# Kernel tuning notes

Measured on AMD Instinct MI355X. Metric: run time of the kernel, lower is better.

The kernel has to match this reference:

```python
import jax, jax.numpy as jnp
import numpy as np


def setup_inputs() -> dict:
    key = jax.random.key(0)
    ks = jax.random.split(key, 6)
    B, T, U = 4, 160, 80
    De, Dd = 640, 640
    inner, vocab = 640, 1024
    return {
        "enc_state": jax.random.normal(ks[0], (B, T, De), jnp.float32),
        "dec_state": jax.random.normal(ks[1], (B, U, Dd), jnp.float32),
        "W1": jax.random.normal(ks[2], (De + Dd, inner), jnp.float32) * (1.0 / np.sqrt(De + Dd)),
        "b1": jax.random.normal(ks[3], (inner,), jnp.float32) * 0.02,
        "W2": jax.random.normal(ks[4], (inner, vocab), jnp.float32) * (1.0 / np.sqrt(inner)),
        "b2": jax.random.normal(ks[5], (vocab,), jnp.float32) * 0.02,
    }


def reference(enc_state, dec_state, W1, b1, W2, b2):
    # Faithful to: cat([enc tiled over U, dec tiled over T], -1) @ W1 + b1,
    # algebraically split so the [B,T,U,2D] concat is never materialized:
    # cat(e, d) @ W1 == e @ W1[:De] + d @ W1[De:]
    De = enc_state.shape[-1]
    W1_enc, W1_dec = W1[:De], W1[De:]
    enc_proj = jnp.einsum("btd,dh->bth", enc_state, W1_enc)   # [B,T,H]
    dec_proj = jnp.einsum("bud,dh->buh", dec_state, W1_dec)   # [B,U,H]
    # broadcast add over the (T,U) lattice -> [B,T,U,H]
    hidden = jnp.tanh(enc_proj[:, :, None, :] + dec_proj[:, None, :, :] + b1)
    logits = jnp.einsum("btuh,hv->btuv", hidden, W2) + b2     # [B,T,U,V]
    return logits
```

## Files before the change

### kernel.cpp

```cpp
#include <hip/hip_runtime.h>
#include <hip/hip_bf16.h>
#include <cstdint>

#define D_    640
#define V_    1024
#define M_    51200

typedef __bf16 bf16x8 __attribute__((ext_vector_type(8)));
typedef float floatx4 __attribute__((ext_vector_type(4)));

__device__ __forceinline__ void g2l16(const void* g, void* l) {
    __builtin_amdgcn_global_load_lds((const __attribute__((address_space(1))) void*)g,
                                     (__attribute__((address_space(3))) void*)l,
                                     16, 0, 0);
}

__device__ __forceinline__ float fast_tanh(float x) {
    float e = __builtin_amdgcn_exp2f(x * 2.8853900817779268f);
    return 1.0f - 2.0f * __builtin_amdgcn_rcpf(e + 1.0f);
}

__global__ __launch_bounds__(256) void proj_kernel(
    const float* __restrict__ enc, const float* __restrict__ dec,
    const float* __restrict__ W1,
    float* __restrict__ encp, float* __restrict__ decp) {
    __shared__ float As[64][36];
    __shared__ float Ws[32][68];

    const int rt = blockIdx.y;
    const int ct = blockIdx.x;
    const float* Asrc; const float* Wsrc; float* Cdst;
    if (rt < 10) { Asrc = enc + (size_t)rt * 64 * D_;        Wsrc = W1;           Cdst = encp + (size_t)rt * 64 * D_; }
    else         { Asrc = dec + (size_t)(rt - 10) * 64 * D_; Wsrc = W1 + D_ * D_; Cdst = decp + (size_t)(rt - 10) * 64 * D_; }

    const int tid = threadIdx.x;
    const int ar = tid >> 2,  ac = (tid & 3) * 8;
    const int wr2 = tid >> 3, wc2 = (tid & 7) * 8;
    const int tr = tid >> 4,  tc = tid & 15;

    float acc[4][4] = {};
    for (int k0 = 0; k0 < D_; k0 += 32) {
        __syncthreads();
        *(floatx4*)&As[ar][ac]       = *(const floatx4*)&Asrc[(size_t)ar * D_ + k0 + ac];
        *(floatx4*)&As[ar][ac + 4]   = *(const floatx4*)&Asrc[(size_t)ar * D_ + k0 + ac + 4];
        *(floatx4*)&Ws[wr2][wc2]     = *(const floatx4*)&Wsrc[(size_t)(k0 + wr2) * D_ + ct * 64 + wc2];
        *(floatx4*)&Ws[wr2][wc2 + 4] = *(const floatx4*)&Wsrc[(size_t)(k0 + wr2) * D_ + ct * 64 + wc2 + 4];
        __syncthreads();
#pragma unroll
        for (int kk = 0; kk < 32; kk++) {
            floatx4 w = *(const floatx4*)&Ws[kk][tc * 4];
            float a0 = As[tr * 4 + 0][kk], a1 = As[tr * 4 + 1][kk];
            float a2 = As[tr * 4 + 2][kk], a3 = As[tr * 4 + 3][kk];
#pragma unroll
            for (int j = 0; j < 4; j++) {
                acc[0][j] += a0 * w[j]; acc[1][j] += a1 * w[j];
                acc[2][j] += a2 * w[j]; acc[3][j] += a3 * w[j];
            }
        }
    }
#pragma unroll
    for (int i = 0; i < 4; i++) {
        floatx4 v = { acc[i][0], acc[i][1], acc[i][2], acc[i][3] };
        *(floatx4*)&Cdst[(size_t)(tr * 4 + i) * D_ + ct * 64 + tc * 4] = v;
    }
}

__global__ __launch_bounds__(256) void w2t_kernel(
    const float* __restrict__ W2, __bf16* __restrict__ W2t) {
    __shared__ __bf16 tile[32][33];
    const int vt = blockIdx.x;
    const int kt = blockIdx.y;
    const int tx = threadIdx.x & 31, ty = threadIdx.x >> 5;
#pragma unroll
    for (int i = 0; i < 4; i++)
        tile[ty + i * 8][tx] = (__bf16)W2[(size_t)(kt * 32 + ty + i * 8) * V_ + vt * 32 + tx];
    __syncthreads();
#pragma unroll
    for (int i = 0; i < 4; i++)
        W2t[(size_t)(vt * 32 + ty + i * 8) * D_ + kt * 32 + tx] = tile[tx][ty + i * 8];
}

__global__ __launch_bounds__(256, 2) void joint_kernel(
    const float* __restrict__ encp, const float* __restrict__ decp,
    const float* __restrict__ b1, const __bf16* __restrict__ W2t,
    const float* __restrict__ b2, float* __restrict__ C) {
    __shared__ __align__(128) char lds[49152];

    const int bid = blockIdx.x;
    const int swz = (bid & 7) * 200 + (bid >> 3);
    const int mt = swz >> 2, nt = swz & 3;
    const int m0 = mt * 128, n0 = nt * 256;

    const int tid = threadIdx.x;
    const int w = tid >> 6, l = tid & 63;
    const int lr = l & 15, lk = l >> 4;

    char* ldsp = (char*)lds;

    const unsigned bsc = (unsigned)(((tid & 3) ^ ((tid >> 4) & 3)) * 16);
    const char* Wb = (const char*)W2t + (size_t)(n0 + (tid >> 2)) * 1280 + bsc;
    const unsigned bdst = (unsigned)(16384 + tid * 16);

    const int pr = tid >> 1;
    const int kh = (tid & 1) * 16;
    const int R  = m0 + pr;
    const int bt = R / 80;
    const int uu = R - bt * 80;
    const int drw = (bt / 160) * 80 + uu;
    const float* ep = encp + (size_t)bt * D_ + kh;
    const float* dp = decp + (size_t)drw * D_ + kh;
    const float* bp = b1 + kh;
    const int ps = (tid & 1) * 2;
    const unsigned psw = (unsigned)((pr >> 2) & 3);
    const unsigned pw0 = (unsigned)(pr * 64 + ((ps ^ psw) * 16));
    const unsigned pw1 = (unsigned)(pr * 64 + (((ps + 1) ^ psw) * 16));

    const unsigned sx = (unsigned)((lk ^ ((lr >> 2) & 3)) * 16);

    floatx4 acc[8][4] = {};

#define STAGE_B(BUF, T) do { \
    const char* _s = Wb + (size_t)(T) * 64; \
    char* _d = ldsp + bdst + (BUF) * 16384; \
    g2l16(_s,                 _d); \
    g2l16(_s + 64 * 1280,     _d + 4096); \
    g2l16(_s + 128 * 1280,    _d + 8192); \
    g2l16(_s + 192 * 1280,    _d + 12288); \
  } while (0)

#define LOAD_EDC(T) do { \
    const float* _e = ep + (T) * 32; const float* _d = dp + (T) * 32; \
    const float* _c = bp + (T) * 32; \
    _Pragma("unroll") for (int q = 0; q < 4; ++q) { \
      eD[q] = *(const floatx4*)(_e + q * 4); \
      dD[q] = *(const floatx4*)(_d + q * 4); \
      cD[q] = *(const floatx4*)(_c + q * 4); \
    } } while (0)

#define PRODUCE_A(BUF) do { \
    bf16x8 h0, h1; \
    _Pragma("unroll") for (int q = 0; q < 4; ++q) { \
      _Pragma("unroll") for (int i2 = 0; i2 < 4; ++i2) { \
        float t_ = fast_tanh(eD[q][i2] + dD[q][i2] + cD[q][i2]); \
        if (q < 2) h0[q * 4 + i2] = (__bf16)t_; else h1[(q - 2) * 4 + i2] = (__bf16)t_; \
      } } \
    *(bf16x8*)(ldsp + (BUF) * 8192 + pw0) = h0; \
    *(bf16x8*)(ldsp + (BUF) * 8192 + pw1) = h1; \
  } while (0)

    {
        floatx4 eD[4], dD[4], cD[4];
        STAGE_B(0, 0);
        LOAD_EDC(0);
        PRODUCE_A(0);
    }
    __syncthreads();

#pragma unroll 1
    for (int t = 0; t < 20; ++t) {
        const int buf = t & 1, nb = buf ^ 1;
        floatx4 eD[4], dD[4], cD[4];
        if (t < 19) {
            STAGE_B(nb, t + 1);
            LOAD_EDC(t + 1);
        }
        bf16x8 af[8], bfr[4];
#pragma unroll
        for (int i = 0; i < 8; ++i)
            af[i] = *(const bf16x8*)(ldsp + buf * 8192 + (i * 16 + lr) * 64 + sx);
#pragma unroll
        for (int j = 0; j < 4; ++j)
            bfr[j] = *(const bf16x8*)(ldsp + 16384 + buf * 16384 + (w * 64 + j * 16 + lr) * 64 + sx);
#pragma unroll
        for (int i = 0; i < 8; ++i)
#pragma unroll
            for (int j = 0; j < 4; ++j)
                acc[i][j] = __builtin_amdgcn_mfma_f32_16x16x32_bf16(af[i], bfr[j], acc[i][j], 0, 0, 0);
        if (t < 19) {
            PRODUCE_A(nb);
        }
        __syncthreads();
    }

#pragma unroll
    for (int j = 0; j < 4; ++j) {
        const int col = n0 + w * 64 + j * 16 + lr;
        const float bj = b2[col];
#pragma unroll
        for (int i = 0; i < 8; ++i) {
            const int row = m0 + i * 16 + lk * 4;
            float* Cp = C + (size_t)row * V_ + col;
#pragma unroll
            for (int rg = 0; rg < 4; ++rg)
                Cp[(size_t)rg * V_] = acc[i][j][rg] + bj;
        }
    }
#undef STAGE_B
#undef LOAD_EDC
#undef PRODUCE_A
}

extern "C" void kernel_launch(void* const* d_in, const int* in_sizes, int n_in,
                              void* d_out, int out_size, void* d_ws, size_t ws_size,
                              hipStream_t stream) {
    const float* enc = (const float*)d_in[0];
    const float* dec = (const float*)d_in[1];
    const float* W1  = (const float*)d_in[2];
    const float* b1  = (const float*)d_in[3];
    const float* W2  = (const float*)d_in[4];
    const float* b2  = (const float*)d_in[5];
    float* out = (float*)d_out;

    char* ws = (char*)d_ws;
    float*  encp = (float*)ws;
    float*  decp = (float*)(ws + 1638400);
    __bf16* W2t  = (__bf16*)(ws + 1638400 + 819200);

    proj_kernel<<<dim3(10, 15), 256, 0, stream>>>(enc, dec, W1, encp, decp);
    w2t_kernel<<<dim3(32, 20), 256, 0, stream>>>(W2, W2t);
    joint_kernel<<<1600, 256, 0, stream>>>(encp, decp, b1, W2t, b2, out);
}
```

Before: 343.6 us.

## Halve joint M tile, double K step, fold b1 into encoder projection

The joint GEMM tile shrinks from 128 to 64 rows, doubling the grid to 3200 blocks, and the K step per iteration grows from 32 to 64. The LDS layout and XOR swizzle are widened to 128-byte rows, and the buffer grows to 80 KB. b1 is now added once in the projection kernel instead of being loaded and added in every joint block. This aims to cut per-iteration barrier overhead and bias traffic, and to give more blocks for latency hiding. In exchange, each output row needs twice as many W2 tile loads per MFMA, and the larger LDS use may limit occupancy.

Measured after the change: 334.7 us. 2.6% less time.

```diff
diff --git a/kernel.cpp b/kernel.cpp
--- a/kernel.cpp
+++ b/kernel.cpp
@@ -22,16 +22,17 @@
 
 __global__ __launch_bounds__(256) void proj_kernel(
     const float* __restrict__ enc, const float* __restrict__ dec,
-    const float* __restrict__ W1,
+    const float* __restrict__ W1, const float* __restrict__ b1,
     float* __restrict__ encp, float* __restrict__ decp) {
     __shared__ float As[64][36];
     __shared__ float Ws[32][68];
 
     const int rt = blockIdx.y;
     const int ct = blockIdx.x;
+    const bool is_enc = (rt < 10);
     const float* Asrc; const float* Wsrc; float* Cdst;
-    if (rt < 10) { Asrc = enc + (size_t)rt * 64 * D_;        Wsrc = W1;           Cdst = encp + (size_t)rt * 64 * D_; }
-    else         { Asrc = dec + (size_t)(rt - 10) * 64 * D_; Wsrc = W1 + D_ * D_; Cdst = decp + (size_t)(rt - 10) * 64 * D_; }
+    if (is_enc) { Asrc = enc + (size_t)rt * 64 * D_;        Wsrc = W1;           Cdst = encp + (size_t)rt * 64 * D_; }
+    else        { Asrc = dec + (size_t)(rt - 10) * 64 * D_; Wsrc = W1 + D_ * D_; Cdst = decp + (size_t)(rt - 10) * 64 * D_; }
 
     const int tid = threadIdx.x;
     const int ar = tid >> 2,  ac = (tid & 3) * 8;
@@ -58,9 +59,12 @@
             }
         }
     }
+    floatx4 bv = {0.f, 0.f, 0.f, 0.f};
+    if (is_enc) bv = *(const floatx4*)&b1[ct * 64 + tc * 4];
 #pragma unroll
     for (int i = 0; i < 4; i++) {
-        floatx4 v = { acc[i][0], acc[i][1], acc[i][2], acc[i][3] };
+        floatx4 v = { acc[i][0] + bv[0], acc[i][1] + bv[1],
+                      acc[i][2] + bv[2], acc[i][3] + bv[3] };
         *(floatx4*)&Cdst[(size_t)(tr * 4 + i) * D_ + ct * 64 + tc * 4] = v;
     }
 }
@@ -82,14 +86,14 @@
 
 __global__ __launch_bounds__(256, 2) void joint_kernel(
     const float* __restrict__ encp, const float* __restrict__ decp,
-    const float* __restrict__ b1, const __bf16* __restrict__ W2t,
-    const float* __restrict__ b2, float* __restrict__ C) {
-    __shared__ __align__(128) char lds[49152];
+    const __bf16* __restrict__ W2t, const float* __restrict__ b2,
+    float* __restrict__ C) {
+    __shared__ __align__(128) char lds[81920];
 
     const int bid = blockIdx.x;
-    const int swz = (bid & 7) * 200 + (bid >> 3);
+    const int swz = (bid & 7) * 400 + (bid >> 3);
     const int mt = swz >> 2, nt = swz & 3;
-    const int m0 = mt * 128, n0 = nt * 256;
+    const int m0 = mt * 64, n0 = nt * 256;
 
     const int tid = threadIdx.x;
     const int w = tid >> 6, l = tid & 63;
@@ -97,51 +101,49 @@
 
     char* ldsp = (char*)lds;
 
-    const unsigned bsc = (unsigned)(((tid & 3) ^ ((tid >> 4) & 3)) * 16);
-    const char* Wb = (const char*)W2t + (size_t)(n0 + (tid >> 2)) * 1280 + bsc;
-    const unsigned bdst = (unsigned)(16384 + tid * 16);
-
-    const int pr = tid >> 1;
-    const int kh = (tid & 1) * 16;
+    const char* Wb = (const char*)W2t
+        + (size_t)(n0 + (tid >> 3)) * 1280
+        + (unsigned)((((tid & 7) ^ ((tid >> 3) & 7)) * 16));
+    const unsigned bdst = 16384u + (unsigned)tid * 16u;
+
+    const int pr = tid >> 2;
+    const int kq = tid & 3;
     const int R  = m0 + pr;
     const int bt = R / 80;
     const int uu = R - bt * 80;
     const int drw = (bt / 160) * 80 + uu;
-    const float* ep = encp + (size_t)bt * D_ + kh;
-    const float* dp = decp + (size_t)drw * D_ + kh;
-    const float* bp = b1 + kh;
-    const int ps = (tid & 1) * 2;
-    const unsigned psw = (unsigned)((pr >> 2) & 3);
-    const unsigned pw0 = (unsigned)(pr * 64 + ((ps ^ psw) * 16));
-    const unsigned pw1 = (unsigned)(pr * 64 + (((ps + 1) ^ psw) * 16));
-
-    const unsigned sx = (unsigned)((lk ^ ((lr >> 2) & 3)) * 16);
-
-    floatx4 acc[8][4] = {};
+    const float* ep = encp + (size_t)bt * D_ + kq * 16;
+    const float* dp = decp + (size_t)drw * D_ + kq * 16;
+    const unsigned pw0 = (unsigned)(pr * 128 + (((kq * 2)     ^ (pr & 7)) * 16));
+    const unsigned pw1 = (unsigned)(pr * 128 + (((kq * 2 + 1) ^ (pr & 7)) * 16));
+
+    floatx4 acc[4][4] = {};
 
 #define STAGE_B(BUF, T) do { \
-    const char* _s = Wb + (size_t)(T) * 64; \
-    char* _d = ldsp + bdst + (BUF) * 16384; \
-    g2l16(_s,                 _d); \
-    g2l16(_s + 64 * 1280,     _d + 4096); \
-    g2l16(_s + 128 * 1280,    _d + 8192); \
-    g2l16(_s + 192 * 1280,    _d + 12288); \
+    const char* _s = Wb + (size_t)(T) * 128; \
+    char* _d = ldsp + bdst + (BUF) * 32768; \
+    g2l16(_s,           _d); \
+    g2l16(_s +  40960,  _d +  4096); \
+    g2l16(_s +  81920,  _d +  8192); \
+    g2l16(_s + 122880,  _d + 12288); \
+    g2l16(_s + 163840,  _d + 16384); \
+    g2l16(_s + 204800,  _d + 20480); \
+    g2l16(_s + 245760,  _d + 24576); \
+    g2l16(_s + 286720,  _d + 28672); \
   } while (0)
 
-#define LOAD_EDC(T) do { \
-    const float* _e = ep + (T) * 32; const float* _d = dp + (T) * 32; \
-    const float* _c = bp + (T) * 32; \
+#define LOAD_ED(T) do { \
+    const float* _e = ep + (T) * 64; const float* _d = dp + (T) * 64; \
     _Pragma("unroll") for (int q = 0; q < 4; ++q) { \
       eD[q] = *(const floatx4*)(_e + q * 4); \
       dD[q] = *(const floatx4*)(_d + q * 4); \
-      cD[q] = *(const floatx4*)(_c + q * 4); \
     } } while (0)
 
 #define PRODUCE_A(BUF) do { \
     bf16x8 h0, h1; \
     _Pragma("unroll") for (int q = 0; q < 4; ++q) { \
       _Pragma("unroll") for (int i2 = 0; i2 < 4; ++i2) { \
-        float t_ = fast_tanh(eD[q][i2] + dD[q][i2] + cD[q][i2]); \
+        float t_ = fast_tanh(eD[q][i2] + dD[q][i2]); \
         if (q < 2) h0[q * 4 + i2] = (__bf16)t_; else h1[(q - 2) * 4 + i2] = (__bf16)t_; \
       } } \
     *(bf16x8*)(ldsp + (BUF) * 8192 + pw0) = h0; \
@@ -149,34 +151,38 @@
   } while (0)
 
     {
-        floatx4 eD[4], dD[4], cD[4];
+        floatx4 eD[4], dD[4];
         STAGE_B(0, 0);
-        LOAD_EDC(0);
+        LOAD_ED(0);
         PRODUCE_A(0);
     }
     __syncthreads();
 
 #pragma unroll 1
-    for (int t = 0; t < 20; ++t) {
+    for (int t = 0; t < 10; ++t) {
         const int buf = t & 1, nb = buf ^ 1;
-        floatx4 eD[4], dD[4], cD[4];
-        if (t < 19) {
+        floatx4 eD[4], dD[4];
+        if (t < 9) {
             STAGE_B(nb, t + 1);
-            LOAD_EDC(t + 1);
-        }
-        bf16x8 af[8], bfr[4];
-#pragma unroll
-        for (int i = 0; i < 8; ++i)
-            af[i] = *(const bf16x8*)(ldsp + buf * 8192 + (i * 16 + lr) * 64 + sx);
-#pragma unroll
-        for (int j = 0; j < 4; ++j)
-            bfr[j] = *(const bf16x8*)(ldsp + 16384 + buf * 16384 + (w * 64 + j * 16 + lr) * 64 + sx);
-#pragma unroll
-        for (int i = 0; i < 8; ++i)
+            LOAD_ED(t + 1);
+        }
+#pragma unroll
+        for (int s = 0; s < 2; ++s) {
+            const unsigned sx = (unsigned)((((s * 4 + lk) ^ (lr & 7)) * 16));
+            bf16x8 af[4], bfr[4];
+#pragma unroll
+            for (int i = 0; i < 4; ++i)
+                af[i] = *(const bf16x8*)(ldsp + buf * 8192 + (i * 16 + lr) * 128 + sx);
 #pragma unroll
             for (int j = 0; j < 4; ++j)
-                acc[i][j] = __builtin_amdgcn_mfma_f32_16x16x32_bf16(af[i], bfr[j], acc[i][j], 0, 0, 0);
-        if (t < 19) {
+                bfr[j] = *(const bf16x8*)(ldsp + 16384 + buf * 32768 + (w * 64 + j * 16 + lr) * 128 + sx);
+#pragma unroll
+            for (int i = 0; i < 4; ++i)
+#pragma unroll
+                for (int j = 0; j < 4; ++j)
+                    acc[i][j] = __builtin_amdgcn_mfma_f32_16x16x32_bf16(af[i], bfr[j], acc[i][j], 0, 0, 0);
+        }
+        if (t < 9) {
             PRODUCE_A(nb);
         }
         __syncthreads();
@@ -187,7 +193,7 @@
         const int col = n0 + w * 64 + j * 16 + lr;
         const float bj = b2[col];
 #pragma unroll
-        for (int i = 0; i < 8; ++i) {
+        for (int i = 0; i < 4; ++i) {
             const int row = m0 + i * 16 + lk * 4;
             float* Cp = C + (size_t)row * V_ + col;
 #pragma unroll
@@ -196,7 +202,7 @@
         }
     }
 #undef STAGE_B
-#undef LOAD_EDC
+#undef LOAD_ED
 #undef PRODUCE_A
 }
 
@@ -216,7 +222,7 @@
     float*  decp = (float*)(ws + 1638400);
     __bf16* W2t  = (__bf16*)(ws + 1638400 + 819200);
 
-    proj_kernel<<<dim3(10, 15), 256, 0, stream>>>(enc, dec, W1, encp, decp);
+    proj_kernel<<<dim3(10, 15), 256, 0, stream>>>(enc, dec, W1, b1, encp, decp);
     w2t_kernel<<<dim3(32, 20), 256, 0, stream>>>(W2, W2t);
-    joint_kernel<<<1600, 256, 0, stream>>>(encp, decp, b1, W2t, b2, out);
-}
+    joint_kernel<<<3200, 256, 0, stream>>>(encp, decp, W2t, b2, out);
+}
```
